# Performance work log

Measured on AMD Instinct MI355X. Metric: run time of the kernel, lower is better.

Reference implementation:

```python
import jax, jax.numpy as jnp
import numpy as np

N = 100_000   # nodes
IN = 256      # input feature size
H = 128       # hidden dim
OUT = 16      # output classes
R = 5         # relations
E = 100_000   # edges per relation
B = 2         # bases


def setup_inputs() -> dict:
    key = jax.random.key(0)
    ks = jax.random.split(key, 10)
    return {
        "x": jax.random.normal(ks[0], (N, IN), jnp.float32),
        "src": jax.random.randint(ks[1], (R, E), 0, N, dtype=jnp.int32),
        "dst": jax.random.randint(ks[2], (R, E), 0, N, dtype=jnp.int32),
        "w_embed": jax.random.normal(ks[3], (IN, H), jnp.float32) / np.sqrt(IN).astype(np.float32),
        "b_embed": jnp.zeros((H,), jnp.float32),
        "basis1": jax.random.normal(ks[4], (B, H, H), jnp.float32) / np.sqrt(H).astype(np.float32),
        "coef1": jax.random.normal(ks[5], (R, B), jnp.float32),
        "bias1": jnp.zeros((H,), jnp.float32),
        "basis2": jax.random.normal(ks[6], (B, H, OUT), jnp.float32) / np.sqrt(H).astype(np.float32),
        "coef2": jax.random.normal(ks[7], (R, B), jnp.float32),
        "bias2": jnp.zeros((OUT,), jnp.float32),
    }


def _rgcn_layer(h, src, dst, basis, coef, bias):
    # basis decomposition: W_r = sum_b coef[r,b] * V_b  -> [R, in, out]
    W = jnp.einsum('rb,bio->rio', coef, basis)

    def per_rel(s, d, w):
        msg = h[s] @ w                                        # [E, out] gather + GEMM
        agg = jax.ops.segment_sum(msg, d, num_segments=N)     # [N, out] scatter-add
        deg = jax.ops.segment_sum(jnp.ones((E,), h.dtype), d, num_segments=N)
        return agg / jnp.maximum(deg, 1.0)[:, None]           # fn.mean per relation

    out = jax.vmap(per_rel)(src, dst, W).sum(axis=0)          # 'sum' cross-relation reduce
    return out + bias


def reference(x, src, dst, w_embed, b_embed, basis1, coef1, bias1, basis2, coef2, bias2):
    h = x @ w_embed + b_embed                                 # EmbeddingLayer (Linear per ntype)
    h = jax.nn.relu(_rgcn_layer(h, src, dst, basis1, coef1, bias1))  # hidden RGCN layer, relu
    return _rgcn_layer(h, src, dst, basis2, coef2, bias2)     # output layer, no activation
```

## Files before the change

kernel.cpp:

```cpp
#include <hip/hip_runtime.h>
#include <hip/hip_bf16.h>
#include <cstddef>
#include <cstdint>

namespace {

constexpr int N = 100000;
constexpr int IN = 256;
constexpr int H = 128;
constexpr int R = 5;
constexpr int E = 100000;
constexpr int RE = R * E;
constexpr int NB = (N + 255) / 256;

using short8 = __attribute__((ext_vector_type(8))) short;
using f32x4 = __attribute__((ext_vector_type(4))) float;

__device__ __forceinline__ float b2f(unsigned int u16) {
  union { unsigned int i; float f; } v;
  v.i = u16 << 16;
  return v.f;
}
__device__ __forceinline__ unsigned short f2b(float f) {
  union { float f; unsigned int u; } v;
  v.f = f;
  unsigned int r = v.u + 0x7fffu + ((v.u >> 16) & 1u);
  return (unsigned short)(r >> 16);
}

__device__ __forceinline__ void load_lds16(const void* g, void* l) {
  __builtin_amdgcn_global_load_lds(
      (const __attribute__((address_space(1))) void*)g,
      (__attribute__((address_space(3))) void*)l, 16, 0, 0);
}

__device__ __forceinline__ float sel5(int r, float a0, float a1, float a2,
                                      float a3, float a4) {
  return r == 0 ? a0 : (r == 1 ? a1 : (r == 2 ? a2 : (r == 3 ? a3 : a4)));
}

__global__ void deg_count(const int* __restrict__ dst, float* __restrict__ deg,
                          int* __restrict__ degtot) {
  int i = blockIdx.x * 256 + threadIdx.x;
  if (i < RE) {
    int d = dst[i];
    atomicAdd(&deg[(i / E) * N + d], 1.0f);
    atomicAdd(&degtot[d], 1);
  }
}

__global__ void inv_deg_k(float* __restrict__ deg) {
  int i = blockIdx.x * 256 + threadIdx.x;
  if (i < R * N) deg[i] = 1.0f / fmaxf(deg[i], 1.0f);
}

__global__ void scan_blk(const int* __restrict__ in, int* __restrict__ part,
                         int* __restrict__ bsum, int n) {
  __shared__ int tmp[256];
  int tid = threadIdx.x;
  int gid = blockIdx.x * 256 + tid;
  int v = (gid < n) ? in[gid] : 0;
  tmp[tid] = v;
  __syncthreads();
  for (int o = 1; o < 256; o <<= 1) {
    int t = (tid >= o) ? tmp[tid - o] : 0;
    __syncthreads();
    tmp[tid] += t;
    __syncthreads();
  }
  if (gid < n) part[gid] = tmp[tid] - v;
  if (tid == 255) bsum[blockIdx.x] = tmp[255];
}

__global__ void scan_top(const int* __restrict__ bsum, int* __restrict__ bscan, int nb) {
  __shared__ int tmp[512];
  int tid = threadIdx.x;
  int v = (tid < nb) ? bsum[tid] : 0;
  tmp[tid] = v;
  __syncthreads();
  for (int o = 1; o < 512; o <<= 1) {
    int t = (tid >= o) ? tmp[tid - o] : 0;
    __syncthreads();
    tmp[tid] += t;
    __syncthreads();
  }
  if (tid < nb) bscan[tid] = tmp[tid] - v;
}

__global__ void scan_add(int* __restrict__ part, const int* __restrict__ bscan, int n) {
  int gid = blockIdx.x * 256 + threadIdx.x;
  if (gid < n) part[gid] += bscan[gid >> 8];
}

__global__ void fill_csr(const int* __restrict__ src, const int* __restrict__ dst,
                         const int* __restrict__ off, int* __restrict__ cursor,
                         int* __restrict__ epk) {
  int i = blockIdx.x * 256 + threadIdx.x;
  if (i >= RE) return;
  int r = i / E;
  int d = dst[i];
  int slot = off[d] + atomicAdd(&cursor[d], 1);
  epk[slot] = src[i] | (r << 20);
}

__global__ void pack_all(const float* __restrict__ w_embed,
                         const float* __restrict__ basis1,
                         const float* __restrict__ basis2,
                         unsigned short* __restrict__ wp1,
                         unsigned short* __restrict__ wpB1,
                         unsigned short* __restrict__ wpB2) {
  int i = blockIdx.x * 256 + threadIdx.x;
  if (i < 32768) {
    int ii = i & 7, lane = (i >> 3) & 63, fb = i >> 9;
    int kc = fb >> 3, ct = fb & 7;
    int k = kc * 32 + ((lane >> 4) << 3) + ii, col = (ct << 4) + (lane & 15);
    wp1[i] = f2b(w_embed[(size_t)k * 128 + col]);
  } else if (i < 65536) {
    int j = i - 32768;
    int ii = j & 7, lane = (j >> 3) & 63, fb = j >> 9;
    int kc = fb >> 3, ct = fb & 7;
    int k = kc * 32 + ((lane >> 4) << 3) + ii, col = (ct << 4) + (lane & 15);
    wpB1[j] = f2b(basis1[(size_t)k * 128 + col]);
  } else if (i < 65536 + 4096) {
    int j = i - 65536;
    int ii = j & 7, lane = (j >> 3) & 63, fb = j >> 9;
    int kc = fb >> 1, ct = fb & 1;
    int k = kc * 32 + ((lane >> 4) << 3) + ii;
    wpB2[j] = f2b(basis2[((size_t)ct * 128 + k) * 16 + (lane & 15)]);
  }
}

__global__ __launch_bounds__(256) void gemm_embed(
    const float* __restrict__ x, const unsigned short* __restrict__ wpack,
    const float* __restrict__ bias, unsigned short* __restrict__ C) {
  __shared__ __align__(16) float alds[4][16][264];
  const int tid = threadIdx.x, lane = tid & 63, wv = tid >> 6;
  const int base = blockIdx.x * 64 + wv * 16;
  if (base >= N) return;
  const int r = lane & 15, g = lane >> 4;
  const short8* wfrag = (const short8*)wpack;

#pragma unroll
  for (int i = 0; i < 16; ++i)
    load_lds16(x + (size_t)(base + i) * IN + lane * 4, &alds[wv][i][0]);

  asm volatile("s_waitcnt vmcnt(0)" ::: "memory");
  __builtin_amdgcn_sched_barrier(0);

  f32x4 acc[8];
#pragma unroll
  for (int ct = 0; ct < 8; ++ct) acc[ct] = (f32x4){0.f, 0.f, 0.f, 0.f};

#pragma unroll
  for (int kc = 0; kc < 8; ++kc) {
    float4 v0 = *(const float4*)&alds[wv][r][kc * 32 + g * 8];
    float4 v1 = *(const float4*)&alds[wv][r][kc * 32 + g * 8 + 4];
    short8 af;
    af[0] = (short)f2b(v0.x); af[1] = (short)f2b(v0.y);
    af[2] = (short)f2b(v0.z); af[3] = (short)f2b(v0.w);
    af[4] = (short)f2b(v1.x); af[5] = (short)f2b(v1.y);
    af[6] = (short)f2b(v1.z); af[7] = (short)f2b(v1.w);
#pragma unroll
    for (int ct = 0; ct < 8; ++ct)
      acc[ct] = __builtin_amdgcn_mfma_f32_16x16x32_bf16(
          af, wfrag[(kc * 8 + ct) * 64 + lane], acc[ct], 0, 0, 0);
  }

#pragma unroll
  for (int ct = 0; ct < 8; ++ct) {
    int col = ct * 16 + r;
    float bs = bias[col];
#pragma unroll
    for (int i = 0; i < 4; ++i)
      C[(size_t)(base + g * 4 + i) * H + col] = f2b(acc[ct][i] + bs);
  }
}

__global__ __launch_bounds__(256) void gemm_fused(
    const unsigned short* __restrict__ u, const unsigned short* __restrict__ wp1,
    const float* __restrict__ bias1, const unsigned short* __restrict__ wp2,
    unsigned short* __restrict__ q) {
  __shared__ __align__(16) unsigned short ust[4][8][520];
  __shared__ __align__(16) unsigned short hl[4][16][136];
  const int tid = threadIdx.x, lane = tid & 63, wv = tid >> 6;
  const int base = blockIdx.x * 64 + wv * 16;
  if (base >= N) return;
  const int r = lane & 15, g = lane >> 4;
  const short8* wf1 = (const short8*)wp1;
  const short8* wf2 = (const short8*)wp2;

#pragma unroll
  for (int p = 0; p < 8; ++p)
    load_lds16(u + (size_t)(base + 2 * p) * 256 + lane * 8, &ust[wv][p][0]);

  asm volatile("s_waitcnt vmcnt(0)" ::: "memory");
  __builtin_amdgcn_sched_barrier(0);

  f32x4 acc[8];
#pragma unroll
  for (int ct = 0; ct < 8; ++ct) acc[ct] = (f32x4){0.f, 0.f, 0.f, 0.f};

#pragma unroll
  for (int kc = 0; kc < 8; ++kc) {
    short8 af = *(const short8*)&ust[wv][r >> 1][(r & 1) * 256 + kc * 32 + g * 8];
#pragma unroll
    for (int ct = 0; ct < 8; ++ct)
      acc[ct] = __builtin_amdgcn_mfma_f32_16x16x32_bf16(
          af, wf1[(kc * 8 + ct) * 64 + lane], acc[ct], 0, 0, 0);
  }

#pragma unroll
  for (int ct = 0; ct < 8; ++ct) {
    int col = ct * 16 + r;
    float bs = bias1[col];
#pragma unroll
    for (int i = 0; i < 4; ++i)
      hl[wv][g * 4 + i][col] = f2b(fmaxf(acc[ct][i] + bs, 0.f));
  }

  asm volatile("s_waitcnt lgkmcnt(0)" ::: "memory");
  __builtin_amdgcn_sched_barrier(0);

  f32x4 acc2[2];
#pragma unroll
  for (int ct = 0; ct < 2; ++ct) acc2[ct] = (f32x4){0.f, 0.f, 0.f, 0.f};

#pragma unroll
  for (int kc = 0; kc < 4; ++kc) {
    short8 af = *(const short8*)&hl[wv][r][kc * 32 + g * 8];
#pragma unroll
    for (int ct = 0; ct < 2; ++ct)
      acc2[ct] = __builtin_amdgcn_mfma_f32_16x16x32_bf16(
          af, wf2[(kc * 2 + ct) * 64 + lane], acc2[ct], 0, 0, 0);
  }

#pragma unroll
  for (int ct = 0; ct < 2; ++ct) {
    int col = ct * 16 + r;
#pragma unroll
    for (int i = 0; i < 4; ++i)
      q[(size_t)(base + g * 4 + i) * 32 + col] = f2b(acc2[ct][i]);
  }
}

__global__ __launch_bounds__(256) void gather1(
    const int* __restrict__ off, const int* __restrict__ degtot,
    const int* __restrict__ epk, const float* __restrict__ invdeg,
    const float* __restrict__ coef1, const unsigned short* __restrict__ hbf,
    unsigned int* __restrict__ ubf) {
  int wid = blockIdx.x * 4 + (threadIdx.x >> 6);
  int lane = threadIdx.x & 63;
  if (wid >= N) return;
  int start = off[wid];
  int cnt = degtot[wid];
  float i0 = invdeg[wid], i1 = invdeg[N + wid], i2 = invdeg[2 * N + wid];
  float i3 = invdeg[3 * N + wid], i4 = invdeg[4 * N + wid];
  float x0 = coef1[0] * i0, y0 = coef1[1] * i0;
  float x1 = coef1[2] * i1, y1 = coef1[3] * i1;
  float x2 = coef1[4] * i2, y2 = coef1[5] * i2;
  float x3 = coef1[6] * i3, y3 = coef1[7] * i3;
  float x4 = coef1[8] * i4, y4 = coef1[9] * i4;
  float u0x = 0.f, u0y = 0.f, u1x = 0.f, u1y = 0.f;
  if (cnt > 0) {
    int pk = epk[start];
    int s = pk & 0xFFFFF, rr = pk >> 20;
    unsigned int hv = ((const unsigned int*)(hbf + (size_t)s * 128))[lane];
    for (int j = 1; j < cnt; ++j) {
      int pkn = epk[start + j];
      int sn = pkn & 0xFFFFF, rn = pkn >> 20;
      unsigned int hvn = ((const unsigned int*)(hbf + (size_t)sn * 128))[lane];
      float c0 = sel5(rr, x0, x1, x2, x3, x4);
      float c1 = sel5(rr, y0, y1, y2, y3, y4);
      float hx = b2f(hv & 0xffffu), hy = b2f(hv >> 16);
      u0x = fmaf(c0, hx, u0x); u0y = fmaf(c0, hy, u0y);
      u1x = fmaf(c1, hx, u1x); u1y = fmaf(c1, hy, u1y);
      rr = rn; hv = hvn;
    }
    float c0 = sel5(rr, x0, x1, x2, x3, x4);
    float c1 = sel5(rr, y0, y1, y2, y3, y4);
    float hx = b2f(hv & 0xffffu), hy = b2f(hv >> 16);
    u0x = fmaf(c0, hx, u0x); u0y = fmaf(c0, hy, u0y);
    u1x = fmaf(c1, hx, u1x); u1y = fmaf(c1, hy, u1y);
  }
  unsigned int* ur = ubf + (size_t)wid * 128;
  ur[lane]      = (unsigned int)f2b(u0x) | ((unsigned int)f2b(u0y) << 16);
  ur[64 + lane] = (unsigned int)f2b(u1x) | ((unsigned int)f2b(u1y) << 16);
}

__global__ __launch_bounds__(256) void gather2(
    const int* __restrict__ off, const int* __restrict__ degtot,
    const int* __restrict__ epk, const float* __restrict__ invdeg,
    const float* __restrict__ coef2, const unsigned short* __restrict__ qbf,
    const float* __restrict__ bias2, float* __restrict__ out) {
  int node = blockIdx.x * 16 + (threadIdx.x >> 4);
  int k = threadIdx.x & 15;
  if (node >= N) return;
  int start = off[node];
  int cnt = degtot[node];
  float i0 = invdeg[node], i1 = invdeg[N + node], i2 = invdeg[2 * N + node];
  float i3 = invdeg[3 * N + node], i4 = invdeg[4 * N + node];
  float x0 = coef2[0] * i0, y0 = coef2[1] * i0;
  float x1 = coef2[2] * i1, y1 = coef2[3] * i1;
  float x2 = coef2[4] * i2, y2 = coef2[5] * i2;
  float x3 = coef2[6] * i3, y3 = coef2[7] * i3;
  float x4 = coef2[8] * i4, y4 = coef2[9] * i4;
  float acc = bias2[k];
  for (int j = 0; j < cnt; ++j) {
    int pk = epk[start + j];
    int s = pk & 0xFFFFF, rr = pk >> 20;
    float c0 = sel5(rr, x0, x1, x2, x3, x4);
    float c1 = sel5(rr, y0, y1, y2, y3, y4);
    acc = fmaf(c0, b2f(qbf[(size_t)s * 32 + k]), acc);
    acc = fmaf(c1, b2f(qbf[(size_t)s * 32 + 16 + k]), acc);
  }
  out[(size_t)node * 16 + k] = acc;
}

}

extern "C" void kernel_launch(void* const* d_in, const int* in_sizes, int n_in,
                              void* d_out, int out_size, void* d_ws, size_t ws_size,
                              hipStream_t stream) {
  const float* x       = (const float*)d_in[0];
  const int*   src     = (const int*)d_in[1];
  const int*   dst     = (const int*)d_in[2];
  const float* w_embed = (const float*)d_in[3];
  const float* b_embed = (const float*)d_in[4];
  const float* basis1  = (const float*)d_in[5];
  const float* coef1   = (const float*)d_in[6];
  const float* bias1   = (const float*)d_in[7];
  const float* basis2  = (const float*)d_in[8];
  const float* coef2   = (const float*)d_in[9];
  const float* bias2   = (const float*)d_in[10];
  float* out = (float*)d_out;

  float* invdeg = (float*)d_ws;
  int*   degtot = (int*)(invdeg + (size_t)R * N);
  int*   cursor = degtot + N;
  int*   off    = cursor + N;
  int*   bsum   = off + N;
  int*   bscan  = bsum + 512;
  int*   epk    = bscan + 512;
  unsigned short* wp1  = (unsigned short*)(epk + RE);
  unsigned short* wpB1 = wp1 + 256 * 128;
  unsigned short* wpB2 = wpB1 + 256 * 128;
  unsigned short* h_bf = wpB2 + 128 * 32;
  unsigned short* u_bf = h_bf + (size_t)N * 128;
  unsigned short* q_bf = u_bf + (size_t)N * 256;

  dim3 b256(256);
  hipMemsetAsync(invdeg, 0, (size_t)(R * N + 2 * N) * sizeof(float), stream);

  deg_count<<<(RE + 255) / 256, b256, 0, stream>>>(dst, invdeg, degtot);
  inv_deg_k<<<(R * N + 255) / 256, b256, 0, stream>>>(invdeg);
  scan_blk<<<NB, b256, 0, stream>>>(degtot, off, bsum, N);
  scan_top<<<1, dim3(512), 0, stream>>>(bsum, bscan, NB);
  scan_add<<<NB, b256, 0, stream>>>(off, bscan, N);
  fill_csr<<<(RE + 255) / 256, b256, 0, stream>>>(src, dst, off, cursor, epk);
  pack_all<<<(65536 + 4096 + 255) / 256, b256, 0, stream>>>(
      w_embed, basis1, basis2, wp1, wpB1, wpB2);

  int gblocks = (N / 16 + 3) / 4;
  gemm_embed<<<gblocks, b256, 0, stream>>>(x, wp1, b_embed, h_bf);
  gather1<<<(N + 3) / 4, b256, 0, stream>>>(off, degtot, epk, invdeg, coef1,
                                            h_bf, (unsigned int*)u_bf);
  gemm_fused<<<gblocks, b256, 0, stream>>>(u_bf, wpB1, bias1, wpB2, q_bf);
  gather2<<<(N + 15) / 16, b256, 0, stream>>>(off, degtot, epk, invdeg, coef2,
                                              q_bf, bias2, out);
}
```

Measured before the change: 379.5 us.

## Precompute per-edge coefficients in CSR, drop LDS staging, split gather2 edges

The CSR fill now stores each edge's source and its per-relation coefficient pairs for both layers, pre-scaled by inverse degree. This removes the per-node invdeg loads and the 5-way relation select from both gather kernels. The two GEMM kernels load A rows straight from global into registers instead of going through LDS with global_load_lds. gather1 prefetches two edges ahead, and gather2 uses a full wave per node with four edge lanes reduced by shuffles. The cost is more per-edge memory traffic, since each edge now carries 20 bytes instead of 4.

```diff
diff --git a/kernel.cpp b/kernel.cpp
--- a/kernel.cpp
+++ b/kernel.cpp
@@ -1,7 +1,6 @@
 #include <hip/hip_runtime.h>
 #include <hip/hip_bf16.h>
 #include <cstddef>
-#include <cstdint>
 
 namespace {
 
@@ -26,17 +25,6 @@
   v.f = f;
   unsigned int r = v.u + 0x7fffu + ((v.u >> 16) & 1u);
   return (unsigned short)(r >> 16);
-}
-
-__device__ __forceinline__ void load_lds16(const void* g, void* l) {
-  __builtin_amdgcn_global_load_lds(
-      (const __attribute__((address_space(1))) void*)g,
-      (__attribute__((address_space(3))) void*)l, 16, 0, 0);
-}
-
-__device__ __forceinline__ float sel5(int r, float a0, float a1, float a2,
-                                      float a3, float a4) {
-  return r == 0 ? a0 : (r == 1 ? a1 : (r == 2 ? a2 : (r == 3 ? a3 : a4)));
 }
 
 __global__ void deg_count(const int* __restrict__ dst, float* __restrict__ deg,
@@ -93,14 +81,19 @@
 }
 
 __global__ void fill_csr(const int* __restrict__ src, const int* __restrict__ dst,
-                         const int* __restrict__ off, int* __restrict__ cursor,
-                         int* __restrict__ epk) {
+                         const float* __restrict__ coef1, const float* __restrict__ coef2,
+                         const float* __restrict__ invdeg, const int* __restrict__ off,
+                         int* __restrict__ cursor, int* __restrict__ esrc,
+                         float2* __restrict__ ecA, float2* __restrict__ ecB) {
   int i = blockIdx.x * 256 + threadIdx.x;
   if (i >= RE) return;
   int r = i / E;
   int d = dst[i];
   int slot = off[d] + atomicAdd(&cursor[d], 1);
-  epk[slot] = src[i] | (r << 20);
+  float id = invdeg[r * N + d];
+  esrc[slot] = src[i];
+  ecA[slot] = make_float2(coef1[2 * r] * id, coef1[2 * r + 1] * id);
+  ecB[slot] = make_float2(coef2[2 * r] * id, coef2[2 * r + 1] * id);
 }
 
 __global__ void pack_all(const float* __restrict__ w_embed,
@@ -133,19 +126,20 @@
 __global__ __launch_bounds__(256) void gemm_embed(
     const float* __restrict__ x, const unsigned short* __restrict__ wpack,
     const float* __restrict__ bias, unsigned short* __restrict__ C) {
-  __shared__ __align__(16) float alds[4][16][264];
-  const int tid = threadIdx.x, lane = tid & 63, wv = tid >> 6;
-  const int base = blockIdx.x * 64 + wv * 16;
+  const int tid = threadIdx.x, lane = tid & 63;
+  const int wave = (blockIdx.x * 256 + tid) >> 6;
+  const int base = wave * 16;
   if (base >= N) return;
   const int r = lane & 15, g = lane >> 4;
   const short8* wfrag = (const short8*)wpack;
 
-#pragma unroll
-  for (int i = 0; i < 16; ++i)
-    load_lds16(x + (size_t)(base + i) * IN + lane * 4, &alds[wv][i][0]);
-
-  asm volatile("s_waitcnt vmcnt(0)" ::: "memory");
-  __builtin_amdgcn_sched_barrier(0);
+  const float* arow = x + (size_t)(base + r) * IN + g * 8;
+  float4 a[8][2];
+#pragma unroll
+  for (int kc = 0; kc < 8; ++kc) {
+    a[kc][0] = *(const float4*)(arow + kc * 32);
+    a[kc][1] = *(const float4*)(arow + kc * 32 + 4);
+  }
 
   f32x4 acc[8];
 #pragma unroll
@@ -153,13 +147,11 @@
 
 #pragma unroll
   for (int kc = 0; kc < 8; ++kc) {
-    float4 v0 = *(const float4*)&alds[wv][r][kc * 32 + g * 8];
-    float4 v1 = *(const float4*)&alds[wv][r][kc * 32 + g * 8 + 4];
     short8 af;
-    af[0] = (short)f2b(v0.x); af[1] = (short)f2b(v0.y);
-    af[2] = (short)f2b(v0.z); af[3] = (short)f2b(v0.w);
-    af[4] = (short)f2b(v1.x); af[5] = (short)f2b(v1.y);
-    af[6] = (short)f2b(v1.z); af[7] = (short)f2b(v1.w);
+    af[0] = (short)f2b(a[kc][0].x); af[1] = (short)f2b(a[kc][0].y);
+    af[2] = (short)f2b(a[kc][0].z); af[3] = (short)f2b(a[kc][0].w);
+    af[4] = (short)f2b(a[kc][1].x); af[5] = (short)f2b(a[kc][1].y);
+    af[6] = (short)f2b(a[kc][1].z); af[7] = (short)f2b(a[kc][1].w);
 #pragma unroll
     for (int ct = 0; ct < 8; ++ct)
       acc[ct] = __builtin_amdgcn_mfma_f32_16x16x32_bf16(
@@ -180,21 +172,19 @@
     const unsigned short* __restrict__ u, const unsigned short* __restrict__ wp1,
     const float* __restrict__ bias1, const unsigned short* __restrict__ wp2,
     unsigned short* __restrict__ q) {
-  __shared__ __align__(16) unsigned short ust[4][8][520];
   __shared__ __align__(16) unsigned short hl[4][16][136];
   const int tid = threadIdx.x, lane = tid & 63, wv = tid >> 6;
-  const int base = blockIdx.x * 64 + wv * 16;
+  const int wave = (blockIdx.x * 256 + tid) >> 6;
+  const int base = wave * 16;
   if (base >= N) return;
   const int r = lane & 15, g = lane >> 4;
   const short8* wf1 = (const short8*)wp1;
   const short8* wf2 = (const short8*)wp2;
 
-#pragma unroll
-  for (int p = 0; p < 8; ++p)
-    load_lds16(u + (size_t)(base + 2 * p) * 256 + lane * 8, &ust[wv][p][0]);
-
-  asm volatile("s_waitcnt vmcnt(0)" ::: "memory");
-  __builtin_amdgcn_sched_barrier(0);
+  const unsigned short* arow = u + (size_t)(base + r) * 256 + g * 8;
+  short8 a[8];
+#pragma unroll
+  for (int kc = 0; kc < 8; ++kc) a[kc] = *(const short8*)(arow + kc * 32);
 
   f32x4 acc[8];
 #pragma unroll
@@ -202,11 +192,10 @@
 
 #pragma unroll
   for (int kc = 0; kc < 8; ++kc) {
-    short8 af = *(const short8*)&ust[wv][r >> 1][(r & 1) * 256 + kc * 32 + g * 8];
 #pragma unroll
     for (int ct = 0; ct < 8; ++ct)
       acc[ct] = __builtin_amdgcn_mfma_f32_16x16x32_bf16(
-          af, wf1[(kc * 8 + ct) * 64 + lane], acc[ct], 0, 0, 0);
+          a[kc], wf1[(kc * 8 + ct) * 64 + lane], acc[ct], 0, 0, 0);
   }
 
 #pragma unroll
@@ -245,42 +234,39 @@
 
 __global__ __launch_bounds__(256) void gather1(
     const int* __restrict__ off, const int* __restrict__ degtot,
-    const int* __restrict__ epk, const float* __restrict__ invdeg,
-    const float* __restrict__ coef1, const unsigned short* __restrict__ hbf,
-    unsigned int* __restrict__ ubf) {
+    const int* __restrict__ esrc, const float2* __restrict__ ecA,
+    const unsigned short* __restrict__ hbf, unsigned int* __restrict__ ubf) {
   int wid = blockIdx.x * 4 + (threadIdx.x >> 6);
   int lane = threadIdx.x & 63;
   if (wid >= N) return;
   int start = off[wid];
   int cnt = degtot[wid];
-  float i0 = invdeg[wid], i1 = invdeg[N + wid], i2 = invdeg[2 * N + wid];
-  float i3 = invdeg[3 * N + wid], i4 = invdeg[4 * N + wid];
-  float x0 = coef1[0] * i0, y0 = coef1[1] * i0;
-  float x1 = coef1[2] * i1, y1 = coef1[3] * i1;
-  float x2 = coef1[4] * i2, y2 = coef1[5] * i2;
-  float x3 = coef1[6] * i3, y3 = coef1[7] * i3;
-  float x4 = coef1[8] * i4, y4 = coef1[9] * i4;
   float u0x = 0.f, u0y = 0.f, u1x = 0.f, u1y = 0.f;
-  if (cnt > 0) {
-    int pk = epk[start];
-    int s = pk & 0xFFFFF, rr = pk >> 20;
-    unsigned int hv = ((const unsigned int*)(hbf + (size_t)s * 128))[lane];
-    for (int j = 1; j < cnt; ++j) {
-      int pkn = epk[start + j];
-      int sn = pkn & 0xFFFFF, rn = pkn >> 20;
-      unsigned int hvn = ((const unsigned int*)(hbf + (size_t)sn * 128))[lane];
-      float c0 = sel5(rr, x0, x1, x2, x3, x4);
-      float c1 = sel5(rr, y0, y1, y2, y3, y4);
-      float hx = b2f(hv & 0xffffu), hy = b2f(hv >> 16);
-      u0x = fmaf(c0, hx, u0x); u0y = fmaf(c0, hy, u0y);
-      u1x = fmaf(c1, hx, u1x); u1y = fmaf(c1, hy, u1y);
-      rr = rn; hv = hvn;
+  const unsigned int* hrows = (const unsigned int*)hbf;
+
+  if (cnt == 1) {
+    float2 c = ecA[start];
+    unsigned int hv = hrows[(size_t)esrc[start] * 64 + lane];
+    float hx = b2f(hv & 0xffffu), hy = b2f(hv >> 16);
+    u0x = c.x * hx; u0y = c.x * hy; u1x = c.y * hx; u1y = c.y * hy;
+  } else if (cnt >= 2) {
+    float2 c0 = ecA[start], c1 = ecA[start + 1];
+    unsigned int hv0 = hrows[(size_t)esrc[start] * 64 + lane];
+    unsigned int hv1 = hrows[(size_t)esrc[start + 1] * 64 + lane];
+    for (int j = 2; j < cnt; ++j) {
+      float2 cn = ecA[start + j];
+      unsigned int hvn = hrows[(size_t)esrc[start + j] * 64 + lane];
+      float hx = b2f(hv0 & 0xffffu), hy = b2f(hv0 >> 16);
+      u0x = fmaf(c0.x, hx, u0x); u0y = fmaf(c0.x, hy, u0y);
+      u1x = fmaf(c0.y, hx, u1x); u1y = fmaf(c0.y, hy, u1y);
+      c0 = c1; hv0 = hv1; c1 = cn; hv1 = hvn;
     }
-    float c0 = sel5(rr, x0, x1, x2, x3, x4);
-    float c1 = sel5(rr, y0, y1, y2, y3, y4);
-    float hx = b2f(hv & 0xffffu), hy = b2f(hv >> 16);
-    u0x = fmaf(c0, hx, u0x); u0y = fmaf(c0, hy, u0y);
-    u1x = fmaf(c1, hx, u1x); u1y = fmaf(c1, hy, u1y);
+    float hx = b2f(hv0 & 0xffffu), hy = b2f(hv0 >> 16);
+    u0x = fmaf(c0.x, hx, u0x); u0y = fmaf(c0.x, hy, u0y);
+    u1x = fmaf(c0.y, hx, u1x); u1y = fmaf(c0.y, hy, u1y);
+    hx = b2f(hv1 & 0xffffu); hy = b2f(hv1 >> 16);
+    u0x = fmaf(c1.x, hx, u0x); u0y = fmaf(c1.x, hy, u0y);
+    u1x = fmaf(c1.y, hx, u1x); u1y = fmaf(c1.y, hy, u1y);
   }
   unsigned int* ur = ubf + (size_t)wid * 128;
   ur[lane]      = (unsigned int)f2b(u0x) | ((unsigned int)f2b(u0y) << 16);
@@ -289,31 +275,25 @@
 
 __global__ __launch_bounds__(256) void gather2(
     const int* __restrict__ off, const int* __restrict__ degtot,
-    const int* __restrict__ epk, const float* __restrict__ invdeg,
-    const float* __restrict__ coef2, const unsigned short* __restrict__ qbf,
-    const float* __restrict__ bias2, float* __restrict__ out) {
-  int node = blockIdx.x * 16 + (threadIdx.x >> 4);
-  int k = threadIdx.x & 15;
+    const int* __restrict__ esrc, const float2* __restrict__ ecB,
+    const unsigned short* __restrict__ qbf, const float* __restrict__ bias2,
+    float* __restrict__ out) {
+  int node = blockIdx.x * 4 + (threadIdx.x >> 6);
+  int lane = threadIdx.x & 63;
   if (node >= N) return;
+  int e = lane >> 4, k = lane & 15;
   int start = off[node];
   int cnt = degtot[node];
-  float i0 = invdeg[node], i1 = invdeg[N + node], i2 = invdeg[2 * N + node];
-  float i3 = invdeg[3 * N + node], i4 = invdeg[4 * N + node];
-  float x0 = coef2[0] * i0, y0 = coef2[1] * i0;
-  float x1 = coef2[2] * i1, y1 = coef2[3] * i1;
-  float x2 = coef2[4] * i2, y2 = coef2[5] * i2;
-  float x3 = coef2[6] * i3, y3 = coef2[7] * i3;
-  float x4 = coef2[8] * i4, y4 = coef2[9] * i4;
-  float acc = bias2[k];
-  for (int j = 0; j < cnt; ++j) {
-    int pk = epk[start + j];
-    int s = pk & 0xFFFFF, rr = pk >> 20;
-    float c0 = sel5(rr, x0, x1, x2, x3, x4);
-    float c1 = sel5(rr, y0, y1, y2, y3, y4);
-    acc = fmaf(c0, b2f(qbf[(size_t)s * 32 + k]), acc);
-    acc = fmaf(c1, b2f(qbf[(size_t)s * 32 + 16 + k]), acc);
-  }
-  out[(size_t)node * 16 + k] = acc;
+  float acc = 0.f;
+  for (int j = e; j < cnt; j += 4) {
+    int s = esrc[start + j];
+    float2 c = ecB[start + j];
+    acc = fmaf(c.x, b2f(qbf[(size_t)s * 32 + k]), acc);
+    acc = fmaf(c.y, b2f(qbf[(size_t)s * 32 + 16 + k]), acc);
+  }
+  acc += __shfl_xor(acc, 16);
+  acc += __shfl_xor(acc, 32);
+  if (e == 0) out[(size_t)node * 16 + k] = acc + bias2[k];
 }
 
 }
@@ -334,14 +314,16 @@
   const float* bias2   = (const float*)d_in[10];
   float* out = (float*)d_out;
 
-  float* invdeg = (float*)d_ws;
-  int*   degtot = (int*)(invdeg + (size_t)R * N);
-  int*   cursor = degtot + N;
-  int*   off    = cursor + N;
-  int*   bsum   = off + N;
-  int*   bscan  = bsum + 512;
-  int*   epk    = bscan + 512;
-  unsigned short* wp1  = (unsigned short*)(epk + RE);
+  float*  invdeg = (float*)d_ws;
+  int*    degtot = (int*)(invdeg + (size_t)R * N);
+  int*    cursor = degtot + N;
+  int*    off    = cursor + N;
+  int*    bsum   = off + N;
+  int*    bscan  = bsum + 512;
+  int*    esrc   = bscan + 512;
+  float2* ecA    = (float2*)(esrc + RE);
+  float2* ecB    = ecA + RE;
+  unsigned short* wp1  = (unsigned short*)(ecB + RE);
   unsigned short* wpB1 = wp1 + 256 * 128;
   unsigned short* wpB2 = wpB1 + 256 * 128;
   unsigned short* h_bf = wpB2 + 128 * 32;
@@ -356,15 +338,15 @@
   scan_blk<<<NB, b256, 0, stream>>>(degtot, off, bsum, N);
   scan_top<<<1, dim3(512), 0, stream>>>(bsum, bscan, NB);
   scan_add<<<NB, b256, 0, stream>>>(off, bscan, N);
-  fill_csr<<<(RE + 255) / 256, b256, 0, stream>>>(src, dst, off, cursor, epk);
+  fill_csr<<<(RE + 255) / 256, b256, 0, stream>>>(src, dst, coef1, coef2, invdeg,
+                                                  off, cursor, esrc, ecA, ecB);
   pack_all<<<(65536 + 4096 + 255) / 256, b256, 0, stream>>>(
       w_embed, basis1, basis2, wp1, wpB1, wpB2);
 
   int gblocks = (N / 16 + 3) / 4;
   gemm_embed<<<gblocks, b256, 0, stream>>>(x, wp1, b_embed, h_bf);
-  gather1<<<(N + 3) / 4, b256, 0, stream>>>(off, degtot, epk, invdeg, coef1,
-                                            h_bf, (unsigned int*)u_bf);
+  gather1<<<(N + 3) / 4, b256, 0, stream>>>(off, degtot, esrc, ecA, h_bf,
+                                            (unsigned int*)u_bf);
   gemm_fused<<<gblocks, b256, 0, stream>>>(u_bf, wpB1, bias1, wpB2, q_bf);
-  gather2<<<(N + 15) / 16, b256, 0, stream>>>(off, degtot, epk, invdeg, coef2,
-                                              q_bf, bias2, out);
-}
+  gather2<<<(N + 3) / 4, b256, 0, stream>>>(off, degtot, esrc, ecB, q_bf, bias2, out);
+}
```

New measurement: 395.5 us. +4.2%, slower.
